# Kernel tuning notes

Hardware: AMD Instinct MI355X
Metric: run time of the kernel (lower is better)

The kernel has to match this reference:

```python
import jax, jax.numpy as jnp
import numpy as np
from math import sqrt

B, D, N, L, H, P = 32, 64, 254, 16, 128, 96  # batch, channels, patch_num, patch_len, hidden, pred_len


def positional_encoding(n, d):
    # standard sinusoidal PE, shape (n, d)
    pos = np.arange(n)[:, None].astype(np.float32)
    div = np.exp(np.arange(0, d, 2).astype(np.float32) * (-np.log(10000.0) / d))
    pe = np.zeros((n, d), dtype=np.float32)
    pe[:, 0::2] = np.sin(pos * div)
    pe[:, 1::2] = np.cos(pos * div)
    return jnp.asarray(pe)


def setup_inputs() -> dict:
    key = jax.random.key(0)
    ks = jax.random.split(key, 7)
    s = 0.05
    return {
        "x": jax.random.normal(ks[0], (B, D, N, L), dtype=jnp.float32),
        "W_enc": jax.random.normal(ks[1], (L, H), dtype=jnp.float32) * s,
        "b_enc": jax.random.normal(ks[2], (H,), dtype=jnp.float32) * s,
        "W1": jax.random.normal(ks[3], (L, H), dtype=jnp.float32) * s,
        "b1": jax.random.normal(ks[4], (H,), dtype=jnp.float32) * s,
        "W2": jax.random.normal(ks[5], (H, P), dtype=jnp.float32) * s,
        "b2": jax.random.normal(ks[6], (P,), dtype=jnp.float32) * s,
        "pos_embed": positional_encoding(N, H),  # buffer, not learned
    }


def reference(x, W_enc, b_enc, W1, b1, W2, b2, pos_embed):
    p = x  # detached clone in torch; same values
    # encode patches: (B,D,N,L) @ (L,H) -> (B,D,N,H), plus PE (N,H) broadcast
    c = jnp.einsum("bdnl,lh->bdnh", x, W_enc) + b_enc + pos_embed
    # score_i = sum_j c_i . c_j / sqrt(H)  ==  c_i . (sum_j c_j) / sqrt(H)
    csum = jnp.sum(c, axis=-2, keepdims=True)            # (B,D,1,H)
    score = jnp.sum(c * csum, axis=-1, keepdims=True) / sqrt(H)  # (B,D,N,1)
    weight = score / jnp.sum(jnp.abs(score), axis=-2, keepdims=True)
    pooled = jnp.sum(x * weight, axis=-2)                # (B,D,L)
    # FeedForward (dropout inactive at eval)
    h = jax.nn.leaky_relu(pooled @ W1 + b1, negative_slope=0.2)
    out = h @ W2 + b2                                    # (B,D,P)
    return out.transpose(0, 2, 1), p                     # (B,P,D), (B,D,N,L)
```

## Files before the change

### kernel.cpp

```cpp
#include <hip/hip_runtime.h>
#include <hip/hip_bf16.h>

#define B_ 32
#define D_ 64
#define N_ 254
#define L_ 16
#define H_ 128
#define P_ 96
#define PAIRS (B_*D_)
#define XPAIR (N_*L_)
#define OUT0  (B_*P_*D_)

#define WS_M    128
#define WS_VK   384
#define WS_BW   400
#define WS_BK   416
#define WS_G    432
#define WS_PK   4496
#define WS_KP   4752

__global__ __launch_bounds__(256) void preK(const float* __restrict__ pos,
                                            float* __restrict__ ws) {
    __shared__ float red[256];
    int t = threadIdx.x;
    int h = t & 127, j = t >> 7;
    int n0 = blockIdx.x * 16;
    float acc = 0.f;
    #pragma unroll
    for (int r = 0; r < 8; r++) {
        int n = n0 + j + 2 * r;
        if (n < N_) acc += pos[n * H_ + h];
    }
    red[t] = acc;
    __syncthreads();
    if (t < 128) ws[WS_KP + blockIdx.x * 128 + t] = red[t] + red[t + 128];
}

__global__ __launch_bounds__(128) void pre2b(const float* __restrict__ W_enc,
                                             const float* __restrict__ b_enc,
                                             const float* __restrict__ pos,
                                             float* __restrict__ ws) {
    __shared__ float Ks[128], bL[128], pLDS[128], red[128], red2[128];
    __shared__ float WL[2048];
    int t = threadIdx.x;
    int n = blockIdx.x;

    {
        float b = b_enc[t];
        float s = 254.f * b;
        #pragma unroll
        for (int g = 0; g < 16; g++) s += ws[WS_KP + g * 128 + t];
        Ks[t] = s;
        bL[t] = b;
    }

    if (n < N_) {
        pLDS[t] = pos[n * H_ + t];
        __syncthreads();
        {
            int l = t >> 3, c = t & 7;
            const float* w = W_enc + l * H_ + c * 16;
            const float* p = pLDS + c * 16;
            float s = 0.f;
            #pragma unroll
            for (int i = 0; i < 16; i++) s += p[i] * w[i];
            red[t] = s;
            red2[t] = pLDS[t] * Ks[t];
        }
        __syncthreads();
        if (t < 16) {
            float s = 0.f;
            #pragma unroll
            for (int c = 0; c < 8; c++) s += red[t * 8 + c];
            ws[WS_G + n * 16 + t] = s;
        }
        if (t >= 64) {
            int lane = t - 64;
            float s = red2[lane] + red2[lane + 64];
            for (int off = 32; off; off >>= 1) s += __shfl_down(s, off);
            if (lane == 0) ws[WS_PK + n] = s;
        }
    } else {
        for (int i = t; i < 512; i += 128) {
            float4 v = ((const float4*)W_enc)[i];
            float* p = &WL[i * 4];
            p[0] = v.x; p[1] = v.y; p[2] = v.z; p[3] = v.w;
        }
        __syncthreads();
        #pragma unroll
        for (int e0 = 0; e0 < 2; e0++) {
            int e = e0 * 128 + t;
            int l1 = e >> 4, l2 = e & 15;
            float s = 0.f;
            for (int h = 0; h < H_; h++) s += WL[l1 * H_ + h] * WL[l2 * H_ + h];
            ws[WS_M + e] = s;
        }
        if (t < 16) {
            float s1 = 0.f, s2 = 0.f;
            for (int h = 0; h < H_; h++) {
                float w = WL[t * H_ + h];
                s1 += w * Ks[h];
                s2 += w * bL[h];
            }
            ws[WS_VK + t] = s1;
            ws[WS_BW + t] = s2;
        }
        if (t == 16) {
            float s = 0.f;
            for (int h = 0; h < H_; h++) s += bL[h] * Ks[h];
            ws[WS_BK] = s;
        }
    }
}

__global__ __launch_bounds__(256) void mainker(const float* __restrict__ x,
                                               const float* __restrict__ W1,
                                               const float* __restrict__ b1,
                                               const float* __restrict__ W2,
                                               const float* __restrict__ b2,
                                               const float* __restrict__ ws,
                                               float* __restrict__ out) {
    __shared__ float xf[N_ * 17 + 16];
    __shared__ float red[256];
    __shared__ float scoreS[N_];
    __shared__ float xsS[16], vS[16], pooledS[16], hS[128];
    __shared__ float s0S, denomS;

    int t  = threadIdx.x;
    int bd = blockIdx.x;

    const float4* xv = (const float4*)(x + (size_t)bd * XPAIR);
    float4*       cv = (float4*)(out + OUT0) + (size_t)bd * (XPAIR / 4);
    for (int i = t; i < XPAIR / 4; i += 256) {
        float4 v = xv[i];
        cv[i] = v;
        int idx = i * 4;
        int n = idx >> 4, l = idx & 15;
        float* p = &xf[n * 17 + l];
        p[0] = v.x; p[1] = v.y; p[2] = v.z; p[3] = v.w;
    }
    __syncthreads();

    {
        int l = t & 15, g = t >> 4;
        float s = 0.f;
        for (int n = g; n < N_; n += 16) s += xf[n * 17 + l];
        red[t] = s;
    }
    __syncthreads();
    if (t < 16) {
        float s = 0.f;
        for (int g = 0; g < 16; g++) s += red[g * 16 + t];
        xsS[t] = s;
    }
    __syncthreads();

    if (t < 16) {
        float s = ws[WS_VK + t];
        for (int l2 = 0; l2 < 16; l2++) s += xsS[l2] * ws[WS_M + l2 * 16 + t];
        vS[t] = s;
    } else if (t == 16) {
        float s = ws[WS_BK];
        for (int l = 0; l < 16; l++) s += xsS[l] * ws[WS_BW + l];
        s0S = s;
    }
    __syncthreads();

    if (t < N_) {
        const float* Gn = ws + WS_G + t * 16;
        float s = s0S + ws[WS_PK + t];
        #pragma unroll
        for (int l = 0; l < 16; l++) s += xf[t * 17 + l] * vS[l] + xsS[l] * Gn[l];
        scoreS[t] = s;
    }
    __syncthreads();

    if (t < 64) {
        float s = 0.f;
        for (int n = t; n < N_; n += 64) s += fabsf(scoreS[n]);
        for (int off = 32; off; off >>= 1) s += __shfl_down(s, off);
        if (t == 0) denomS = s;
    }
    __syncthreads();
    float inv = 1.0f / denomS;

    {
        int l = t & 15, g = t >> 4;
        float s = 0.f;
        for (int n = g; n < N_; n += 16) s += xf[n * 17 + l] * scoreS[n];
        red[t] = s;
    }
    __syncthreads();
    if (t < 16) {
        float s = 0.f;
        for (int g = 0; g < 16; g++) s += red[g * 16 + t];
        pooledS[t] = s * inv;
    }
    __syncthreads();

    if (t < 128) {
        float s = b1[t];
        #pragma unroll
        for (int l = 0; l < 16; l++) s += pooledS[l] * W1[l * H_ + t];
        hS[t] = s > 0.f ? s : 0.2f * s;
    }
    __syncthreads();

    if (t < 96) {
        float s = b2[t];
        for (int j = 0; j < 128; j++) s += hS[j] * W2[j * P_ + t];
        int b = bd >> 6, d = bd & 63;
        out[b * (P_ * D_) + t * D_ + d] = s;
    }
}

extern "C" void kernel_launch(void* const* d_in, const int* in_sizes, int n_in,
                              void* d_out, int out_size, void* d_ws, size_t ws_size,
                              hipStream_t stream) {
    const float* x     = (const float*)d_in[0];
    const float* W_enc = (const float*)d_in[1];
    const float* b_enc = (const float*)d_in[2];
    const float* W1    = (const float*)d_in[3];
    const float* b1    = (const float*)d_in[4];
    const float* W2    = (const float*)d_in[5];
    const float* b2    = (const float*)d_in[6];
    const float* pos   = (const float*)d_in[7];
    float* ws  = (float*)d_ws;
    float* out = (float*)d_out;

    hipLaunchKernelGGL(preK,   dim3(16),    dim3(256), 0, stream, pos, ws);
    hipLaunchKernelGGL(pre2b,  dim3(255),   dim3(128), 0, stream, W_enc, b_enc, pos, ws);
    hipLaunchKernelGGL(mainker, dim3(PAIRS), dim3(256), 0, stream, x, W1, b1, W2, b2, ws, out);
}
```

Baseline: 119.6 us.

## Merge precompute kernels, transpose W2, use nontemporal copy and fewer barriers

Folds the two precompute kernels into one launch. A single block now computes the pos-sum K and the per-patch PK dot products, and an extra block transposes W2 into the workspace. The main kernel issues unrolled nontemporal float4 loads and stores for the x passthrough copy. It removes two barriers by using shuffles for the xs/v/s0 reduction and deferring the denominator read. The final projection reads the transposed W2 with vectorized float4 loads. The PK computation is serialized into one block, which may lengthen the precompute critical path.

```diff
diff --git a/kernel.cpp b/kernel.cpp
--- a/kernel.cpp
+++ b/kernel.cpp
@@ -1,5 +1,4 @@
 #include <hip/hip_runtime.h>
-#include <hip/hip_bf16.h>
 
 #define B_ 32
 #define D_ 64
@@ -17,83 +16,71 @@
 #define WS_BK   416
 #define WS_G    432
 #define WS_PK   4496
-#define WS_KP   4752
-
-__global__ __launch_bounds__(256) void preK(const float* __restrict__ pos,
-                                            float* __restrict__ ws) {
-    __shared__ float red[256];
-    int t = threadIdx.x;
-    int h = t & 127, j = t >> 7;
-    int n0 = blockIdx.x * 16;
-    float acc = 0.f;
-    #pragma unroll
-    for (int r = 0; r < 8; r++) {
-        int n = n0 + j + 2 * r;
-        if (n < N_) acc += pos[n * H_ + h];
-    }
-    red[t] = acc;
-    __syncthreads();
-    if (t < 128) ws[WS_KP + blockIdx.x * 128 + t] = red[t] + red[t + 128];
-}
-
-__global__ __launch_bounds__(128) void pre2b(const float* __restrict__ W_enc,
-                                             const float* __restrict__ b_enc,
-                                             const float* __restrict__ pos,
-                                             float* __restrict__ ws) {
-    __shared__ float Ks[128], bL[128], pLDS[128], red[128], red2[128];
-    __shared__ float WL[2048];
+#define WS_W2T  4752
+
+typedef float f32x4 __attribute__((ext_vector_type(4)));
+
+__global__ __launch_bounds__(256) void pre(const float* __restrict__ W_enc,
+                                           const float* __restrict__ b_enc,
+                                           const float* __restrict__ pos,
+                                           const float* __restrict__ W2,
+                                           float* __restrict__ ws) {
     int t = threadIdx.x;
     int n = blockIdx.x;
 
-    {
-        float b = b_enc[t];
-        float s = 254.f * b;
-        #pragma unroll
-        for (int g = 0; g < 16; g++) s += ws[WS_KP + g * 128 + t];
-        Ks[t] = s;
-        bL[t] = b;
-    }
-
     if (n < N_) {
-        pLDS[t] = pos[n * H_ + t];
+        __shared__ float pLDS[128], red[256];
+        if (t < 128) pLDS[t] = pos[n * H_ + t];
         __syncthreads();
         {
-            int l = t >> 3, c = t & 7;
-            const float* w = W_enc + l * H_ + c * 16;
-            const float* p = pLDS + c * 16;
+            int l = t >> 4, c = t & 15;
+            const float* w = W_enc + l * H_ + c * 8;
+            const float* p = pLDS + c * 8;
             float s = 0.f;
             #pragma unroll
-            for (int i = 0; i < 16; i++) s += p[i] * w[i];
+            for (int i = 0; i < 8; i++) s += p[i] * w[i];
             red[t] = s;
-            red2[t] = pLDS[t] * Ks[t];
         }
         __syncthreads();
         if (t < 16) {
             float s = 0.f;
             #pragma unroll
-            for (int c = 0; c < 8; c++) s += red[t * 8 + c];
+            for (int c = 0; c < 16; c++) s += red[t * 16 + c];
             ws[WS_G + n * 16 + t] = s;
         }
-        if (t >= 64) {
-            int lane = t - 64;
-            float s = red2[lane] + red2[lane + 64];
-            for (int off = 32; off; off >>= 1) s += __shfl_down(s, off);
-            if (lane == 0) ws[WS_PK + n] = s;
-        }
-    } else {
-        for (int i = t; i < 512; i += 128) {
+    } else if (n == N_) {
+        __shared__ float WL[2048], Ks[128], bL[128], red[256];
+        for (int i = t; i < 512; i += 256) {
             float4 v = ((const float4*)W_enc)[i];
             float* p = &WL[i * 4];
             p[0] = v.x; p[1] = v.y; p[2] = v.z; p[3] = v.w;
         }
-        __syncthreads();
-        #pragma unroll
-        for (int e0 = 0; e0 < 2; e0++) {
-            int e = e0 * 128 + t;
-            int l1 = e >> 4, l2 = e & 15;
+        {
+            int h = t & 127, half = t >> 7;
+            float s = 0.f;
+            #pragma unroll 4
+            for (int r = half; r < N_; r += 2) s += pos[r * H_ + h];
+            red[t] = s;
+        }
+        __syncthreads();
+        if (t < 128) {
+            float b = b_enc[t];
+            bL[t] = b;
+            Ks[t] = 254.f * b + red[t] + red[t + 128];
+        }
+        __syncthreads();
+        if (t < N_) {
+            const float* pr = pos + t * H_;
+            float s = 0.f;
+            #pragma unroll 8
+            for (int h = 0; h < H_; h++) s += pr[h] * Ks[h];
+            ws[WS_PK + t] = s;
+        }
+        {
+            int l1 = t >> 4, l2 = t & 15;
             float s = 0.f;
             for (int h = 0; h < H_; h++) s += WL[l1 * H_ + h] * WL[l2 * H_ + h];
-            ws[WS_M + e] = s;
+            ws[WS_M + t] = s;
         }
         if (t < 16) {
             float s1 = 0.f, s2 = 0.f;
@@ -110,13 +97,17 @@
             for (int h = 0; h < H_; h++) s += bL[h] * Ks[h];
             ws[WS_BK] = s;
         }
+    } else {
+        for (int i = t; i < H_ * P_; i += 256) {
+            int j = i / P_, p = i - j * P_;
+            ws[WS_W2T + p * H_ + j] = W2[i];
+        }
     }
 }
 
 __global__ __launch_bounds__(256) void mainker(const float* __restrict__ x,
                                                const float* __restrict__ W1,
                                                const float* __restrict__ b1,
-                                               const float* __restrict__ W2,
                                                const float* __restrict__ b2,
                                                const float* __restrict__ ws,
                                                float* __restrict__ out) {
@@ -129,16 +120,26 @@
     int t  = threadIdx.x;
     int bd = blockIdx.x;
 
-    const float4* xv = (const float4*)(x + (size_t)bd * XPAIR);
-    float4*       cv = (float4*)(out + OUT0) + (size_t)bd * (XPAIR / 4);
-    for (int i = t; i < XPAIR / 4; i += 256) {
-        float4 v = xv[i];
-        cv[i] = v;
-        int idx = i * 4;
-        int n = idx >> 4, l = idx & 15;
-        float* p = &xf[n * 17 + l];
-        p[0] = v.x; p[1] = v.y; p[2] = v.z; p[3] = v.w;
-    }
+    const f32x4* xv = (const f32x4*)(x + (size_t)bd * XPAIR);
+    f32x4*       cv = (f32x4*)(out + OUT0) + (size_t)bd * (XPAIR / 4);
+
+    f32x4 v0 = __builtin_nontemporal_load(xv + t);
+    f32x4 v1 = __builtin_nontemporal_load(xv + t + 256);
+    f32x4 v2 = __builtin_nontemporal_load(xv + t + 512);
+    f32x4 v3 = {0.f, 0.f, 0.f, 0.f};
+    bool has3 = (t < 248);
+    if (has3) v3 = __builtin_nontemporal_load(xv + t + 768);
+
+    __builtin_nontemporal_store(v0, cv + t);
+    __builtin_nontemporal_store(v1, cv + t + 256);
+    __builtin_nontemporal_store(v2, cv + t + 512);
+    if (has3) __builtin_nontemporal_store(v3, cv + t + 768);
+
+    #define UNPACK(vv, ii) { int idx = (ii) * 4; float* p = &xf[(idx >> 4) * 17 + (idx & 15)]; \
+                             p[0] = vv[0]; p[1] = vv[1]; p[2] = vv[2]; p[3] = vv[3]; }
+    UNPACK(v0, t); UNPACK(v1, t + 256); UNPACK(v2, t + 512);
+    if (has3) UNPACK(v3, t + 768);
+    #undef UNPACK
     __syncthreads();
 
     {
@@ -148,21 +149,20 @@
         red[t] = s;
     }
     __syncthreads();
+
     if (t < 16) {
-        float s = 0.f;
-        for (int g = 0; g < 16; g++) s += red[g * 16 + t];
-        xsS[t] = s;
-    }
-    __syncthreads();
-
-    if (t < 16) {
+        float xsv = 0.f;
+        #pragma unroll
+        for (int g = 0; g < 16; g++) xsv += red[g * 16 + t];
+        xsS[t] = xsv;
         float s = ws[WS_VK + t];
-        for (int l2 = 0; l2 < 16; l2++) s += xsS[l2] * ws[WS_M + l2 * 16 + t];
+        #pragma unroll
+        for (int l2 = 0; l2 < 16; l2++) s += __shfl(xsv, l2) * ws[WS_M + l2 * 16 + t];
         vS[t] = s;
-    } else if (t == 16) {
-        float s = ws[WS_BK];
-        for (int l = 0; l < 16; l++) s += xsS[l] * ws[WS_BW + l];
-        s0S = s;
+        float s0p = xsv * ws[WS_BW + t];
+        #pragma unroll
+        for (int off = 8; off; off >>= 1) s0p += __shfl_down(s0p, off);
+        if (t == 0) s0S = ws[WS_BK] + s0p;
     }
     __syncthreads();
 
@@ -181,9 +181,6 @@
         for (int off = 32; off; off >>= 1) s += __shfl_down(s, off);
         if (t == 0) denomS = s;
     }
-    __syncthreads();
-    float inv = 1.0f / denomS;
-
     {
         int l = t & 15, g = t >> 4;
         float s = 0.f;
@@ -192,9 +189,11 @@
     }
     __syncthreads();
     if (t < 16) {
-        float s = 0.f;
+        float invd = 1.0f / denomS;
+        float s = 0.f;
+        #pragma unroll
         for (int g = 0; g < 16; g++) s += red[g * 16 + t];
-        pooledS[t] = s * inv;
+        pooledS[t] = s * invd;
     }
     __syncthreads();
 
@@ -208,7 +207,13 @@
 
     if (t < 96) {
         float s = b2[t];
-        for (int j = 0; j < 128; j++) s += hS[j] * W2[j * P_ + t];
+        const float4* w = (const float4*)(ws + WS_W2T + t * H_);
+        #pragma unroll
+        for (int k = 0; k < 32; k++) {
+            float4 wv = w[k];
+            s += hS[4 * k] * wv.x + hS[4 * k + 1] * wv.y
+               + hS[4 * k + 2] * wv.z + hS[4 * k + 3] * wv.w;
+        }
         int b = bd >> 6, d = bd & 63;
         out[b * (P_ * D_) + t * D_ + d] = s;
     }
@@ -228,7 +233,6 @@
     float* ws  = (float*)d_ws;
     float* out = (float*)d_out;
 
-    hipLaunchKernelGGL(preK,   dim3(16),    dim3(256), 0, stream, pos, ws);
-    hipLaunchKernelGGL(pre2b,  dim3(255),   dim3(128), 0, stream, W_enc, b_enc, pos, ws);
-    hipLaunchKernelGGL(mainker, dim3(PAIRS), dim3(256), 0, stream, x, W1, b1, W2, b2, ws, out);
+    hipLaunchKernelGGL(pre,     dim3(256),   dim3(256), 0, stream, W_enc, b_enc, pos, W2, ws);
+    hipLaunchKernelGGL(mainker, dim3(PAIRS), dim3(256), 0, stream, x, W1, b1, b2, ws, out);
 }
```

Result: slower. 140.4 us (+17.3%).
